# Optimization experiments

Hardware: AMD Instinct MI355X
Metric: run time of the kernel (lower is better)

Reference implementation:

```python
import jax, jax.numpy as jnp
import numpy as np

N = 50000      # nodes
E = 800000     # edges
D_IN = 128     # in_channels == hidden_channels
D_H = 128
R = 4          # num_relations
L = 3          # n_layers
D_MID = D_H // 4
D_OUT = 40
BN_EPS = 1e-5


def setup_inputs() -> dict:
    key = jax.random.key(0)
    ks = jax.random.split(key, 12)
    return {
        "x": jax.random.normal(ks[0], (N, D_IN), dtype=jnp.float32),
        "edge_index": jax.random.randint(ks[1], (2, E), 0, N, dtype=jnp.int64),
        "edge_type": jax.random.randint(ks[2], (E,), 0, R, dtype=jnp.int64),
        "W_skip": jax.random.normal(ks[3], (L, D_IN, D_H), dtype=jnp.float32) * 0.1,
        "W_film_skip": jax.random.normal(ks[4], (L, D_IN, 2 * D_H), dtype=jnp.float32) * 0.1,
        "W_rel": jax.random.normal(ks[5], (L, R, D_IN, D_H), dtype=jnp.float32) * 0.1,
        "W_film": jax.random.normal(ks[6], (L, R, D_IN, 2 * D_H), dtype=jnp.float32) * 0.1,
        "bn_w": jnp.ones((L, D_H), dtype=jnp.float32),
        "bn_b": jnp.zeros((L, D_H), dtype=jnp.float32),
        "lin1_w": jax.random.normal(ks[7], (D_H, D_MID), dtype=jnp.float32) * 0.1,
        "lin1_b": jnp.zeros((D_MID,), dtype=jnp.float32),
        "lin2_w": jax.random.normal(ks[8], (D_MID, D_OUT), dtype=jnp.float32) * 0.1,
        "lin2_b": jnp.zeros((D_OUT,), dtype=jnp.float32),
    }


def _film_conv(x, Wsk, Wfsk, Wr, Wf, src, dst, etype):
    # Self path: FiLM-modulated skip transform (PyG FiLMConv, act=ReLU).
    beta_s, gamma_s = jnp.split(x @ Wfsk, 2, axis=-1)  # split order: beta, gamma
    out = jax.nn.relu(gamma_s * (x @ Wsk) + beta_s)    # [N, D_H]
    # Per-relation node transforms (small GEMMs, avoids dynamic edge masking).
    xr = jnp.einsum('ni,rio->nro', x, Wr)              # [N, R, D_H]
    bg = jnp.einsum('ni,rio->nro', x, Wf)              # [N, R, 2*D_H]
    beta, gamma = jnp.split(bg, 2, axis=-1)            # each [N, R, D_H]
    # Messages: gamma_i * (W_r x_j) + beta_i, relation chosen per edge.
    msg = jax.nn.relu(gamma[dst, etype] * xr[src, etype] + beta[dst, etype])  # [E, D_H]
    # Mean aggregation per (target node, relation) subgraph, then sum relations.
    seg = dst * R + etype
    sums = jax.ops.segment_sum(msg, seg, num_segments=N * R)
    cnts = jax.ops.segment_sum(jnp.ones((msg.shape[0],), msg.dtype), seg, num_segments=N * R)
    mean = sums / jnp.maximum(cnts, 1.0)[:, None]      # [N*R, D_H]
    return out + mean.reshape(N, R, D_H).sum(axis=1)


def _batchnorm(h, w, b):
    mu = h.mean(axis=0)
    var = ((h - mu) ** 2).mean(axis=0)  # biased variance, as torch BN training
    return (h - mu) * jax.lax.rsqrt(var + BN_EPS) * w + b


def reference(x, edge_index, edge_type, W_skip, W_film_skip, W_rel, W_film,
              bn_w, bn_b, lin1_w, lin1_b, lin2_w, lin2_b):
    src, dst = edge_index[0], edge_index[1]
    h = x
    for l in range(L):
        h = _film_conv(h, W_skip[l], W_film_skip[l], W_rel[l], W_film[l], src, dst, edge_type)
        h = _batchnorm(h, bn_w[l], bn_b[l])
        # dropout treated as identity (deterministic reference)
    h = jax.nn.leaky_relu(h @ lin1_w + lin1_b, negative_slope=0.2)
    return h @ lin2_w + lin2_b
```

## Files before the change

### kernel.cpp

```cpp
#include <hip/hip_runtime.h>

#define N_NODES 50000
#define N_EDGES 800000
#define D 128
#define R_REL 4
#define L_LAYERS 3
#define M_SEG (N_NODES * R_REL)
#define NCOLS 384
#define BN_EPS 1e-5f

typedef unsigned short u16;
typedef __attribute__((ext_vector_type(8))) short short8v;
typedef __attribute__((ext_vector_type(4))) float f32x4;

static __device__ __forceinline__ u16 f2b(float f) {
    union { float f; unsigned int u; } a; a.f = f;
    unsigned int u = a.u;
    return (u16)((u + 0x7FFFu + ((u >> 16) & 1u)) >> 16);
}
static __device__ __forceinline__ float b2f(u16 b) {
    union { unsigned int u; float f; } a; a.u = ((unsigned int)b) << 16;
    return a.f;
}

__global__ void pack_w(const float* __restrict__ Wsk, const float* __restrict__ Wfsk,
                       const float* __restrict__ Wr, const float* __restrict__ Wf,
                       u16* __restrict__ Wpb) {
    int idx = blockIdx.x * 256 + threadIdx.x;
    if (idx >= L_LAYERS * 5 * NCOLS * D) return;
    int k = idx & 127;
    int rem = idx >> 7;
    int j = rem % NCOLS;
    int lp = rem / NCOLS;
    int l = lp / 5, p = lp % 5;
    float v;
    if (p == 0) {
        v = (j < D) ? Wsk[(l * D + k) * D + j] : Wfsk[(l * D + k) * 2 * D + (j - D)];
    } else {
        int r = p - 1;
        v = (j < D) ? Wr[((l * R_REL + r) * D + k) * D + j]
                    : Wf[((l * R_REL + r) * D + k) * 2 * D + (j - D)];
    }
    Wpb[idx] = f2b(v);
}

__global__ void cvt_bf16(const float* __restrict__ x, u16* __restrict__ xb) {
    int idx = blockIdx.x * 256 + threadIdx.x;
    if (idx >= N_NODES * D) return;
    xb[idx] = f2b(x[idx]);
}

__global__ void hist_k(const int* __restrict__ dst, const int* __restrict__ et, int* __restrict__ cnt) {
    int e = blockIdx.x * 256 + threadIdx.x;
    if (e >= N_EDGES) return;
    atomicAdd(&cnt[dst[e] * R_REL + et[e]], 1);
}

__global__ void scan_a(const int* __restrict__ cnt, int* __restrict__ bsum) {
    __shared__ int sm[256];
    int t = threadIdx.x;
    int idx = blockIdx.x * 256 + t;
    sm[t] = (idx < M_SEG) ? cnt[idx] : 0;
    __syncthreads();
    for (int s = 128; s > 0; s >>= 1) {
        if (t < s) sm[t] += sm[t + s];
        __syncthreads();
    }
    if (t == 0) bsum[blockIdx.x] = sm[0];
}

#define NB_SCAN 782
__global__ void scan_b(const int* __restrict__ bsum, int* __restrict__ bsumex, int* __restrict__ offs) {
    __shared__ int sm[1024];
    int t = threadIdx.x;
    int v = (t < NB_SCAN) ? bsum[t] : 0;
    sm[t] = v;
    __syncthreads();
    for (int d = 1; d < 1024; d <<= 1) {
        int add = (t >= d) ? sm[t - d] : 0;
        __syncthreads();
        sm[t] += add;
        __syncthreads();
    }
    if (t < NB_SCAN) bsumex[t] = sm[t] - v;
    if (t == NB_SCAN - 1) offs[M_SEG] = sm[t];
}

__global__ void scan_c(const int* __restrict__ cnt, const int* __restrict__ bsumex, int* __restrict__ offs) {
    __shared__ int sm[256];
    int t = threadIdx.x;
    int idx = blockIdx.x * 256 + t;
    int v = (idx < M_SEG) ? cnt[idx] : 0;
    sm[t] = v;
    __syncthreads();
    for (int d = 1; d < 256; d <<= 1) {
        int add = (t >= d) ? sm[t - d] : 0;
        __syncthreads();
        sm[t] += add;
        __syncthreads();
    }
    if (idx < M_SEG) offs[idx] = bsumex[blockIdx.x] + sm[t] - v;
}

__global__ void scatter_k(const int* __restrict__ src, const int* __restrict__ dst,
                          const int* __restrict__ et, const int* __restrict__ offs,
                          int* __restrict__ tmp, int* __restrict__ esrc) {
    int e = blockIdx.x * 256 + threadIdx.x;
    if (e >= N_EDGES) return;
    int seg = dst[e] * R_REL + et[e];
    int pos = offs[seg] + atomicAdd(&tmp[seg], 1);
    esrc[pos] = src[e];
}

__global__ __launch_bounds__(512) void gemm5(const uint4* __restrict__ Aq,
                                             const uint4* __restrict__ Bq,
                                             u16* __restrict__ Call) {
    __shared__ uint4 As[128 * 16];
    int t = threadIdx.x;
    int m0 = blockIdx.x * 128;
    int p = blockIdx.y;
#pragma unroll
    for (int i = 0; i < 4; ++i) {
        int idx = i * 512 + t;
        int row = idx >> 4, kk = idx & 15;
        int gr = m0 + row;
        if (gr >= N_NODES) gr = N_NODES - 1;
        As[(row << 4) + (kk ^ (row & 7))] = Aq[gr * 16 + kk];
    }
    __syncthreads();
    int lane = t & 63, w = t >> 6;
    int wr = w >> 2, wc = w & 3;
    int lr = lane & 15, lh = lane >> 4;
    short8v a[4][4];
#pragma unroll
    for (int m = 0; m < 4; ++m) {
        int row = wr * 64 + m * 16 + lr;
#pragma unroll
        for (int ks = 0; ks < 4; ++ks)
            a[m][ks] = *reinterpret_cast<const short8v*>(&As[(row << 4) + ((ks * 4 + lh) ^ (row & 7))]);
    }
    const uint4* Bp = Bq + (size_t)p * NCOLS * 16;
    u16* Cp = Call + (size_t)p * N_NODES * NCOLS;
    f32x4 zero = {0.f, 0.f, 0.f, 0.f};
#pragma unroll
    for (int chunk = 0; chunk < 3; ++chunk) {
        int n0 = chunk * 128;
        f32x4 acc[4][2];
#pragma unroll
        for (int m = 0; m < 4; ++m)
#pragma unroll
            for (int n = 0; n < 2; ++n) acc[m][n] = zero;
#pragma unroll
        for (int ks = 0; ks < 4; ++ks) {
            short8v b[2];
#pragma unroll
            for (int n = 0; n < 2; ++n) {
                int row = n0 + wc * 32 + n * 16 + lr;
                b[n] = *reinterpret_cast<const short8v*>(&Bp[row * 16 + ks * 4 + lh]);
            }
#pragma unroll
            for (int m = 0; m < 4; ++m)
#pragma unroll
                for (int n = 0; n < 2; ++n)
                    acc[m][n] = __builtin_amdgcn_mfma_f32_16x16x32_bf16(a[m][ks], b[n], acc[m][n], 0, 0, 0);
        }
#pragma unroll
        for (int m = 0; m < 4; ++m) {
#pragma unroll
            for (int reg = 0; reg < 4; ++reg) {
                int gr = m0 + wr * 64 + m * 16 + lh * 4 + reg;
                if (gr < N_NODES) {
#pragma unroll
                    for (int n = 0; n < 2; ++n) {
                        int col = n0 + wc * 32 + n * 16 + lr;
                        Cp[(size_t)gr * NCOLS + col] = f2b(acc[m][n][reg]);
                    }
                }
            }
        }
    }
}

__global__ __launch_bounds__(256) void film_agg2(const u16* __restrict__ bufAll,
                                                 const int* __restrict__ offs, const int* __restrict__ esrc,
                                                 float* __restrict__ acc) {
    int t = threadIdx.x;
    int n = blockIdx.x * 4 + (t >> 6);
    int lane = t & 63;
    int cg = (lane & 31) * 4;
    int half = lane >> 5;
    const u16* rowS = bufAll + (size_t)n * NCOLS;
    ushort4 xs = *reinterpret_cast<const ushort4*>(&rowS[cg]);
    ushort4 bs = *reinterpret_cast<const ushort4*>(&rowS[128 + cg]);
    ushort4 gs = *reinterpret_cast<const ushort4*>(&rowS[256 + cg]);
    float h0 = fmaxf(b2f(gs.x) * b2f(xs.x) + b2f(bs.x), 0.f);
    float h1 = fmaxf(b2f(gs.y) * b2f(xs.y) + b2f(bs.y), 0.f);
    float h2 = fmaxf(b2f(gs.z) * b2f(xs.z) + b2f(bs.z), 0.f);
    float h3 = fmaxf(b2f(gs.w) * b2f(xs.w) + b2f(bs.w), 0.f);
#pragma unroll
    for (int r = 0; r < R_REL; ++r) {
        const u16* B = bufAll + (size_t)(1 + r) * N_NODES * NCOLS;
        int seg = n * R_REL + r;
        int beg = offs[seg], end = offs[seg + 1];
        if (beg < end) {
            const u16* grow = B + (size_t)n * NCOLS;
            ushort4 b4 = *reinterpret_cast<const ushort4*>(&grow[128 + cg]);
            ushort4 g4 = *reinterpret_cast<const ushort4*>(&grow[256 + cg]);
            float g0 = b2f(g4.x), g1 = b2f(g4.y), g2 = b2f(g4.z), g3 = b2f(g4.w);
            float be0 = b2f(b4.x), be1 = b2f(b4.y), be2 = b2f(b4.z), be3 = b2f(b4.w);
            float s0 = 0.f, s1 = 0.f, s2 = 0.f, s3 = 0.f;
            for (int i = beg + half; i < end; i += 2) {
                int src = esrc[i];
                ushort4 x4 = *reinterpret_cast<const ushort4*>(&B[(size_t)src * NCOLS + cg]);
                s0 += fmaxf(g0 * b2f(x4.x) + be0, 0.f);
                s1 += fmaxf(g1 * b2f(x4.y) + be1, 0.f);
                s2 += fmaxf(g2 * b2f(x4.z) + be2, 0.f);
                s3 += fmaxf(g3 * b2f(x4.w) + be3, 0.f);
            }
            s0 += __shfl_xor(s0, 32);
            s1 += __shfl_xor(s1, 32);
            s2 += __shfl_xor(s2, 32);
            s3 += __shfl_xor(s3, 32);
            float inv = 1.f / (float)(end - beg);
            h0 += s0 * inv; h1 += s1 * inv; h2 += s2 * inv; h3 += s3 * inv;
        }
    }
    if (half == 0) {
        float4 o = make_float4(h0, h1, h2, h3);
        *reinterpret_cast<float4*>(&acc[(size_t)n * D + cg]) = o;
    }
}

__global__ __launch_bounds__(256) void bn_stats2(const float* __restrict__ acc, float* __restrict__ sums) {
    __shared__ float sm[256], sm2[256];
    int t = threadIdx.x;
    int c = t & 127, half = t >> 7;
    int rows = (N_NODES + gridDim.x - 1) / gridDim.x;
    int nb = blockIdx.x * rows;
    int n1 = min(nb + rows, N_NODES);
    float s = 0.f, s2 = 0.f;
    for (int n = nb + half; n < n1; n += 2) {
        float v = acc[n * D + c];
        s += v;
        s2 += v * v;
    }
    sm[t] = s; sm2[t] = s2;
    __syncthreads();
    if (t < 128) {
        atomicAdd(&sums[c], sm[t] + sm[t + 128]);
        atomicAdd(&sums[128 + c], sm2[t] + sm2[t + 128]);
    }
}

__global__ void bn_apply(const float* __restrict__ acc, const float* __restrict__ sums,
                         const float* __restrict__ w, const float* __restrict__ b,
                         u16* __restrict__ hb16) {
    int idx = blockIdx.x * 256 + threadIdx.x;
    if (idx >= N_NODES * D) return;
    int c = idx & 127;
    const float invn = 1.f / (float)N_NODES;
    float mu = sums[c] * invn;
    float var = sums[128 + c] * invn - mu * mu;
    float rs = rsqrtf(var + BN_EPS);
    hb16[idx] = f2b((acc[idx] - mu) * rs * w[c] + b[c]);
}

__global__ __launch_bounds__(128) void head_k(const u16* __restrict__ h, const float* __restrict__ w1,
                                              const float* __restrict__ b1, const float* __restrict__ w2,
                                              const float* __restrict__ b2, float* __restrict__ out) {
    __shared__ float hrow[128];
    __shared__ float part[128];
    __shared__ float mid[32];
    int n = blockIdx.x, t = threadIdx.x;
    hrow[t] = b2f(h[n * D + t]);
    __syncthreads();
    int m = t & 31, q = t >> 5;
    float p = 0.f;
#pragma unroll 8
    for (int k = q * 32; k < q * 32 + 32; ++k) p += hrow[k] * w1[k * 32 + m];
    part[t] = p;
    __syncthreads();
    if (t < 32) {
        float v = part[t] + part[t + 32] + part[t + 64] + part[t + 96] + b1[t];
        mid[t] = v > 0.f ? v : 0.2f * v;
    }
    __syncthreads();
    if (t < 40) {
        float o = b2[t];
#pragma unroll 8
        for (int mm = 0; mm < 32; ++mm) o += mid[mm] * w2[mm * 40 + t];
        out[n * 40 + t] = o;
    }
}

extern "C" void kernel_launch(void* const* d_in, const int* in_sizes, int n_in,
                              void* d_out, int out_size, void* d_ws, size_t ws_size,
                              hipStream_t stream) {
    const float* x    = (const float*)d_in[0];
    const int*   ei   = (const int*)d_in[1];
    const int*   et   = (const int*)d_in[2];
    const float* Wsk  = (const float*)d_in[3];
    const float* Wfsk = (const float*)d_in[4];
    const float* Wr   = (const float*)d_in[5];
    const float* Wf   = (const float*)d_in[6];
    const float* bnw  = (const float*)d_in[7];
    const float* bnb  = (const float*)d_in[8];
    const float* w1   = (const float*)d_in[9];
    const float* b1   = (const float*)d_in[10];
    const float* w2   = (const float*)d_in[11];
    const float* b2   = (const float*)d_in[12];
    const int* src = ei;
    const int* dst = ei + N_EDGES;

    char* ws = (char*)d_ws;
    size_t off = 0;
    auto alloc = [&](size_t bytes) -> void* {
        void* p = ws + off;
        off += (bytes + 255) & ~(size_t)255;
        return p;
    };
    u16*   Wpb  = (u16*)alloc((size_t)L_LAYERS * 5 * NCOLS * D * 2);
    u16*   inb  = (u16*)alloc((size_t)N_NODES * D * 2);
    float* acc  = (float*)alloc((size_t)N_NODES * D * 4);
    int*   cnt    = (int*)alloc((size_t)M_SEG * 4);
    int*   tmp    = (int*)alloc((size_t)M_SEG * 4);
    float* bns    = (float*)alloc((size_t)L_LAYERS * 256 * 4);
    int*   offs   = (int*)alloc((size_t)(M_SEG + 1) * 4);
    int*   esrc   = (int*)alloc((size_t)N_EDGES * 4);
    int*   bsum   = (int*)alloc(1024 * 4);
    int*   bsumex = (int*)alloc(1024 * 4);
    u16*   bufAll = (u16*)alloc((size_t)5 * N_NODES * NCOLS * 2);

    hipMemsetAsync(cnt, 0, (size_t)M_SEG * 8 + (size_t)L_LAYERS * 1024, stream);

    pack_w<<<(L_LAYERS * 5 * NCOLS * D + 255) / 256, 256, 0, stream>>>(Wsk, Wfsk, Wr, Wf, Wpb);
    cvt_bf16<<<(N_NODES * D + 255) / 256, 256, 0, stream>>>(x, inb);
    hist_k<<<(N_EDGES + 255) / 256, 256, 0, stream>>>(dst, et, cnt);
    scan_a<<<NB_SCAN, 256, 0, stream>>>(cnt, bsum);
    scan_b<<<1, 1024, 0, stream>>>(bsum, bsumex, offs);
    scan_c<<<NB_SCAN, 256, 0, stream>>>(cnt, bsumex, offs);
    scatter_k<<<(N_EDGES + 255) / 256, 256, 0, stream>>>(src, dst, et, offs, tmp, esrc);

    const int nbm = (N_NODES + 127) / 128;
    for (int l = 0; l < L_LAYERS; ++l) {
        gemm5<<<dim3(nbm, 5), 512, 0, stream>>>((const uint4*)inb,
                                                (const uint4*)(Wpb + (size_t)(l * 5) * NCOLS * D), bufAll);
        film_agg2<<<N_NODES / 4, 256, 0, stream>>>(bufAll, offs, esrc, acc);
        bn_stats2<<<256, 256, 0, stream>>>(acc, bns + l * 256);
        bn_apply<<<(N_NODES * D + 255) / 256, 256, 0, stream>>>(acc, bns + l * 256, bnw + l * D, bnb + l * D, inb);
    }
    head_k<<<N_NODES, 128, 0, stream>>>(inb, w1, b1, w2, b2, (float*)d_out);
}
```

Before: 836.1 us.

## Split self-path GEMM with fused FiLM epilogue, stage GEMM output via LDS

The skip-path GEMM moves into its own kernel, which applies the FiLM modulation and ReLU in registers and writes only the 128-wide result instead of three 128-column planes. The relation GEMM now stages its output tile through swizzled shared memory so global stores are 16-byte coalesced rather than scattered 2-byte writes. Edge ranks are recorded during the histogram, so the scatter step no longer needs a second atomic pass or the tmp buffer. The cost is an extra kernel launch per layer, an extra rank array, and 32KB more LDS per block, which may lower occupancy.

```diff
diff --git a/kernel.cpp b/kernel.cpp
--- a/kernel.cpp
+++ b/kernel.cpp
@@ -50,10 +50,11 @@
     xb[idx] = f2b(x[idx]);
 }
 
-__global__ void hist_k(const int* __restrict__ dst, const int* __restrict__ et, int* __restrict__ cnt) {
+__global__ void hist_k(const int* __restrict__ dst, const int* __restrict__ et,
+                       int* __restrict__ cnt, int* __restrict__ rank) {
     int e = blockIdx.x * 256 + threadIdx.x;
     if (e >= N_EDGES) return;
-    atomicAdd(&cnt[dst[e] * R_REL + et[e]], 1);
+    rank[e] = atomicAdd(&cnt[dst[e] * R_REL + et[e]], 1);
 }
 
 __global__ void scan_a(const int* __restrict__ cnt, int* __restrict__ bsum) {
@@ -104,18 +105,18 @@
 
 __global__ void scatter_k(const int* __restrict__ src, const int* __restrict__ dst,
                           const int* __restrict__ et, const int* __restrict__ offs,
-                          int* __restrict__ tmp, int* __restrict__ esrc) {
+                          const int* __restrict__ rank, int* __restrict__ esrc) {
     int e = blockIdx.x * 256 + threadIdx.x;
     if (e >= N_EDGES) return;
     int seg = dst[e] * R_REL + et[e];
-    int pos = offs[seg] + atomicAdd(&tmp[seg], 1);
-    esrc[pos] = src[e];
-}
-
-__global__ __launch_bounds__(512) void gemm5(const uint4* __restrict__ Aq,
-                                             const uint4* __restrict__ Bq,
-                                             u16* __restrict__ Call) {
+    esrc[offs[seg] + rank[e]] = src[e];
+}
+
+__global__ __launch_bounds__(512) void gemm_planes(const uint4* __restrict__ Aq,
+                                                   const uint4* __restrict__ Bq,
+                                                   u16* __restrict__ bufR) {
     __shared__ uint4 As[128 * 16];
+    __shared__ u16 Cs[128 * 128];
     int t = threadIdx.x;
     int m0 = blockIdx.x * 128;
     int p = blockIdx.y;
@@ -139,9 +140,10 @@
         for (int ks = 0; ks < 4; ++ks)
             a[m][ks] = *reinterpret_cast<const short8v*>(&As[(row << 4) + ((ks * 4 + lh) ^ (row & 7))]);
     }
-    const uint4* Bp = Bq + (size_t)p * NCOLS * 16;
-    u16* Cp = Call + (size_t)p * N_NODES * NCOLS;
+    const uint4* Bp = Bq + (size_t)(1 + p) * NCOLS * 16;
+    u16* Cp = bufR + (size_t)p * N_NODES * NCOLS;
     f32x4 zero = {0.f, 0.f, 0.f, 0.f};
+    int srow = t >> 4, sslot = t & 15;
 #pragma unroll
     for (int chunk = 0; chunk < 3; ++chunk) {
         int n0 = chunk * 128;
@@ -164,24 +166,123 @@
                 for (int n = 0; n < 2; ++n)
                     acc[m][n] = __builtin_amdgcn_mfma_f32_16x16x32_bf16(a[m][ks], b[n], acc[m][n], 0, 0, 0);
         }
-#pragma unroll
-        for (int m = 0; m < 4; ++m) {
+        __syncthreads();
+#pragma unroll
+        for (int m = 0; m < 4; ++m)
 #pragma unroll
             for (int reg = 0; reg < 4; ++reg) {
-                int gr = m0 + wr * 64 + m * 16 + lh * 4 + reg;
-                if (gr < N_NODES) {
+                int row = wr * 64 + m * 16 + lh * 4 + reg;
+#pragma unroll
+                for (int n = 0; n < 2; ++n) {
+                    int col = wc * 32 + n * 16 + lr;
+                    Cs[row * 128 + (col ^ ((lh & 1) << 4))] = f2b(acc[m][n][reg]);
+                }
+            }
+        __syncthreads();
+#pragma unroll
+        for (int it = 0; it < 4; ++it) {
+            int row = it * 32 + srow;
+            int gr = m0 + row;
+            if (gr < N_NODES) {
+                uint4 v = *reinterpret_cast<const uint4*>(
+                    &Cs[row * 128 + ((sslot * 8) ^ (((row >> 2) & 1) << 4))]);
+                *reinterpret_cast<uint4*>(&Cp[(size_t)gr * NCOLS + n0 + sslot * 8]) = v;
+            }
+        }
+    }
+}
+
+__global__ __launch_bounds__(512) void gemm_self(const uint4* __restrict__ Aq,
+                                                 const uint4* __restrict__ Bq,
+                                                 u16* __restrict__ selfb) {
+    __shared__ uint4 As[128 * 16];
+    __shared__ u16 Cs[128 * 128];
+    int t = threadIdx.x;
+    int m0 = blockIdx.x * 128;
+#pragma unroll
+    for (int i = 0; i < 4; ++i) {
+        int idx = i * 512 + t;
+        int row = idx >> 4, kk = idx & 15;
+        int gr = m0 + row;
+        if (gr >= N_NODES) gr = N_NODES - 1;
+        As[(row << 4) + (kk ^ (row & 7))] = Aq[gr * 16 + kk];
+    }
+    __syncthreads();
+    int lane = t & 63, w = t >> 6;
+    int wr = w >> 2, wc = w & 3;
+    int lr = lane & 15, lh = lane >> 4;
+    short8v a[4][4];
+#pragma unroll
+    for (int m = 0; m < 4; ++m) {
+        int row = wr * 64 + m * 16 + lr;
+#pragma unroll
+        for (int ks = 0; ks < 4; ++ks)
+            a[m][ks] = *reinterpret_cast<const short8v*>(&As[(row << 4) + ((ks * 4 + lh) ^ (row & 7))]);
+    }
+    f32x4 zero = {0.f, 0.f, 0.f, 0.f};
+    f32x4 hx[4][2], hb[4][2];
+#pragma unroll
+    for (int chunk = 0; chunk < 3; ++chunk) {
+        int n0 = chunk * 128;
+        f32x4 acc[4][2];
+#pragma unroll
+        for (int m = 0; m < 4; ++m)
+#pragma unroll
+            for (int n = 0; n < 2; ++n) acc[m][n] = zero;
+#pragma unroll
+        for (int ks = 0; ks < 4; ++ks) {
+            short8v b[2];
+#pragma unroll
+            for (int n = 0; n < 2; ++n) {
+                int row = n0 + wc * 32 + n * 16 + lr;
+                b[n] = *reinterpret_cast<const short8v*>(&Bq[row * 16 + ks * 4 + lh]);
+            }
+#pragma unroll
+            for (int m = 0; m < 4; ++m)
+#pragma unroll
+                for (int n = 0; n < 2; ++n)
+                    acc[m][n] = __builtin_amdgcn_mfma_f32_16x16x32_bf16(a[m][ks], b[n], acc[m][n], 0, 0, 0);
+        }
+        if (chunk == 0) {
+#pragma unroll
+            for (int m = 0; m < 4; ++m)
+#pragma unroll
+                for (int n = 0; n < 2; ++n) hx[m][n] = acc[m][n];
+        } else if (chunk == 1) {
+#pragma unroll
+            for (int m = 0; m < 4; ++m)
+#pragma unroll
+                for (int n = 0; n < 2; ++n) hb[m][n] = acc[m][n];
+        } else {
+#pragma unroll
+            for (int m = 0; m < 4; ++m)
+#pragma unroll
+                for (int reg = 0; reg < 4; ++reg) {
+                    int row = wr * 64 + m * 16 + lh * 4 + reg;
 #pragma unroll
                     for (int n = 0; n < 2; ++n) {
-                        int col = n0 + wc * 32 + n * 16 + lr;
-                        Cp[(size_t)gr * NCOLS + col] = f2b(acc[m][n][reg]);
+                        int col = wc * 32 + n * 16 + lr;
+                        float h = fmaxf(acc[m][n][reg] * hx[m][n][reg] + hb[m][n][reg], 0.f);
+                        Cs[row * 128 + (col ^ ((lh & 1) << 4))] = f2b(h);
                     }
                 }
-            }
-        }
-    }
-}
-
-__global__ __launch_bounds__(256) void film_agg2(const u16* __restrict__ bufAll,
+        }
+    }
+    __syncthreads();
+    int srow = t >> 4, sslot = t & 15;
+#pragma unroll
+    for (int it = 0; it < 4; ++it) {
+        int row = it * 32 + srow;
+        int gr = m0 + row;
+        if (gr < N_NODES) {
+            uint4 v = *reinterpret_cast<const uint4*>(
+                &Cs[row * 128 + ((sslot * 8) ^ (((row >> 2) & 1) << 4))]);
+            *reinterpret_cast<uint4*>(&selfb[(size_t)gr * D + sslot * 8]) = v;
+        }
+    }
+}
+
+__global__ __launch_bounds__(256) void film_agg2(const u16* __restrict__ selfb, const u16* __restrict__ bufR,
                                                  const int* __restrict__ offs, const int* __restrict__ esrc,
                                                  float* __restrict__ acc) {
     int t = threadIdx.x;
@@ -189,17 +290,11 @@
     int lane = t & 63;
     int cg = (lane & 31) * 4;
     int half = lane >> 5;
-    const u16* rowS = bufAll + (size_t)n * NCOLS;
-    ushort4 xs = *reinterpret_cast<const ushort4*>(&rowS[cg]);
-    ushort4 bs = *reinterpret_cast<const ushort4*>(&rowS[128 + cg]);
-    ushort4 gs = *reinterpret_cast<const ushort4*>(&rowS[256 + cg]);
-    float h0 = fmaxf(b2f(gs.x) * b2f(xs.x) + b2f(bs.x), 0.f);
-    float h1 = fmaxf(b2f(gs.y) * b2f(xs.y) + b2f(bs.y), 0.f);
-    float h2 = fmaxf(b2f(gs.z) * b2f(xs.z) + b2f(bs.z), 0.f);
-    float h3 = fmaxf(b2f(gs.w) * b2f(xs.w) + b2f(bs.w), 0.f);
+    ushort4 hs = *reinterpret_cast<const ushort4*>(&selfb[(size_t)n * D + cg]);
+    float h0 = b2f(hs.x), h1 = b2f(hs.y), h2 = b2f(hs.z), h3 = b2f(hs.w);
 #pragma unroll
     for (int r = 0; r < R_REL; ++r) {
-        const u16* B = bufAll + (size_t)(1 + r) * N_NODES * NCOLS;
+        const u16* B = bufR + (size_t)r * N_NODES * NCOLS;
         int seg = n * R_REL + r;
         int beg = offs[seg], end = offs[seg + 1];
         if (beg < end) {
@@ -323,29 +418,32 @@
     u16*   inb  = (u16*)alloc((size_t)N_NODES * D * 2);
     float* acc  = (float*)alloc((size_t)N_NODES * D * 4);
     int*   cnt    = (int*)alloc((size_t)M_SEG * 4);
-    int*   tmp    = (int*)alloc((size_t)M_SEG * 4);
     float* bns    = (float*)alloc((size_t)L_LAYERS * 256 * 4);
     int*   offs   = (int*)alloc((size_t)(M_SEG + 1) * 4);
     int*   esrc   = (int*)alloc((size_t)N_EDGES * 4);
+    int*   rank   = (int*)alloc((size_t)N_EDGES * 4);
     int*   bsum   = (int*)alloc(1024 * 4);
     int*   bsumex = (int*)alloc(1024 * 4);
-    u16*   bufAll = (u16*)alloc((size_t)5 * N_NODES * NCOLS * 2);
-
-    hipMemsetAsync(cnt, 0, (size_t)M_SEG * 8 + (size_t)L_LAYERS * 1024, stream);
+    u16*   bufR   = (u16*)alloc((size_t)4 * N_NODES * NCOLS * 2);
+    u16*   selfb  = (u16*)alloc((size_t)N_NODES * D * 2);
+
+    hipMemsetAsync(cnt, 0, (size_t)M_SEG * 4 + (size_t)L_LAYERS * 1024, stream);
 
     pack_w<<<(L_LAYERS * 5 * NCOLS * D + 255) / 256, 256, 0, stream>>>(Wsk, Wfsk, Wr, Wf, Wpb);
     cvt_bf16<<<(N_NODES * D + 255) / 256, 256, 0, stream>>>(x, inb);
-    hist_k<<<(N_EDGES + 255) / 256, 256, 0, stream>>>(dst, et, cnt);
+    hist_k<<<(N_EDGES + 255) / 256, 256, 0, stream>>>(dst, et, cnt, rank);
     scan_a<<<NB_SCAN, 256, 0, stream>>>(cnt, bsum);
     scan_b<<<1, 1024, 0, stream>>>(bsum, bsumex, offs);
     scan_c<<<NB_SCAN, 256, 0, stream>>>(cnt, bsumex, offs);
-    scatter_k<<<(N_EDGES + 255) / 256, 256, 0, stream>>>(src, dst, et, offs, tmp, esrc);
+    scatter_k<<<(N_EDGES + 255) / 256, 256, 0, stream>>>(src, dst, et, offs, rank, esrc);
 
     const int nbm = (N_NODES + 127) / 128;
     for (int l = 0; l < L_LAYERS; ++l) {
-        gemm5<<<dim3(nbm, 5), 512, 0, stream>>>((const uint4*)inb,
-                                                (const uint4*)(Wpb + (size_t)(l * 5) * NCOLS * D), bufAll);
-        film_agg2<<<N_NODES / 4, 256, 0, stream>>>(bufAll, offs, esrc, acc);
+        const uint4* Aq = (const uint4*)inb;
+        const uint4* Wl = (const uint4*)(Wpb + (size_t)(l * 5) * NCOLS * D);
+        gemm_planes<<<dim3(nbm, 4), 512, 0, stream>>>(Aq, Wl, bufR);
+        gemm_self<<<dim3(nbm, 1), 512, 0, stream>>>(Aq, Wl, selfb);
+        film_agg2<<<N_NODES / 4, 256, 0, stream>>>(selfb, bufR, offs, esrc, acc);
         bn_stats2<<<256, 256, 0, stream>>>(acc, bns + l * 256);
         bn_apply<<<(N_NODES * D + 255) / 256, 256, 0, stream>>>(acc, bns + l * 256, bnw + l * D, bnb + l * D, inb);
     }
```

Result: faster. 799.0 us (-4.4%).
